# Performance work log

Hardware: AMD Instinct MI355X
Metric: run time of the kernel (lower is better)

The kernel has to match this reference:

```python
import jax, jax.numpy as jnp
import numpy as np

EMBED = 128
HIDDEN = 256
N_NODES = 50000
N_EDGES = 640000
LN_EPS = 1e-5


def setup_inputs() -> dict:
    key = jax.random.key(0)
    ks = jax.random.split(key, 10)
    node_embeddings = jax.random.normal(ks[0], (N_NODES, EMBED), dtype=jnp.float32)
    edge_embeddings = jax.random.normal(ks[1], (N_EDGES, EMBED), dtype=jnp.float32)
    edge_index_list = jax.random.randint(ks[2], (2, N_EDGES), 0, N_NODES, dtype=jnp.int64 if jax.config.jax_enable_x64 else jnp.int32)
    # LayerNorm params
    ln_gamma = jnp.ones((EMBED,), dtype=jnp.float32)
    ln_beta = jnp.zeros((EMBED,), dtype=jnp.float32)
    # phi: Linear(embed->hidden), Linear(hidden->embed); xavier-ish init
    W1 = jax.random.normal(ks[3], (EMBED, HIDDEN), dtype=jnp.float32) * (1.0 / np.sqrt(EMBED))
    b1 = jnp.zeros((HIDDEN,), dtype=jnp.float32)
    W2 = jax.random.normal(ks[4], (HIDDEN, EMBED), dtype=jnp.float32) * (1.0 / np.sqrt(HIDDEN))
    b2 = jnp.zeros((EMBED,), dtype=jnp.float32)
    # theta: Linear(embed->embed)
    Wt = jax.random.normal(ks[5], (EMBED, EMBED), dtype=jnp.float32) * (1.0 / np.sqrt(EMBED))
    bt = jnp.zeros((EMBED,), dtype=jnp.float32)
    return {
        "node_embeddings": node_embeddings,
        "edge_embeddings": edge_embeddings,
        "edge_index_list": edge_index_list,
        "ln_gamma": ln_gamma, "ln_beta": ln_beta,
        "W1": W1, "b1": b1, "W2": W2, "b2": b2,
        "Wt": Wt, "bt": bt,
    }


def _layer_norm(x, gamma, beta):
    mu = jnp.mean(x, axis=-1, keepdims=True)
    var = jnp.var(x, axis=-1, keepdims=True)
    return (x - mu) * jax.lax.rsqrt(var + LN_EPS) * gamma + beta


def reference(node_embeddings, edge_embeddings, edge_index_list,
              ln_gamma, ln_beta, W1, b1, W2, b2, Wt, bt):
    n_nodes = node_embeddings.shape[0]
    h = _layer_norm(node_embeddings, ln_gamma, ln_beta)  # [N, D]
    center = edge_index_list[0]    # [E]
    neighbor = edge_index_list[1]  # [E]
    h_c = h[center]                # [E, D] gather
    h_n = h[neighbor]              # [E, D] gather
    s = edge_embeddings + h_c + h_n  # [E, D]
    # phi: SiLU -> Linear -> SiLU -> Linear
    t = jax.nn.silu(s) @ W1 + b1          # [E, H]
    theta_edge = jax.nn.silu(t) @ W2 + b2  # [E, D]
    msg = h_n * theta_edge                 # [E, D]
    agg = jax.ops.segment_sum(msg, center, num_segments=n_nodes)  # [N, D]
    # theta: SiLU -> Linear
    out = jax.nn.silu(h + agg) @ Wt + bt   # [N, D]
    return out
```

## Files before the change

### kernel.cpp

```cpp
#include <hip/hip_runtime.h>
#include <hip/hip_bf16.h>
#include <stdint.h>

#define EMBED 128
#define HIDDEN 256

typedef __bf16 v8bf __attribute__((ext_vector_type(8)));
typedef float v4f __attribute__((ext_vector_type(4)));

__device__ __forceinline__ float bf2f(unsigned short u){
    union { uint32_t i; float f; } v; v.i = ((uint32_t)u) << 16; return v.f;
}
__device__ __forceinline__ unsigned short f2bf(float f){
    __hip_bfloat16 b = __float2bfloat16(f);
    union { __hip_bfloat16 b; unsigned short u; } cv; cv.b = b; return cv.u;
}
__device__ __forceinline__ uint32_t pack2(float a, float b){
    __hip_bfloat162 t = __float22bfloat162_rn(make_float2(a, b));
    union { __hip_bfloat162 v; uint32_t u; } cv; cv.v = t; return cv.u;
}
__device__ __forceinline__ float lo_f(uint32_t u){ union{uint32_t i;float f;}v; v.i=u<<16; return v.f; }
__device__ __forceinline__ float hi_f(uint32_t u){ union{uint32_t i;float f;}v; v.i=u&0xffff0000u; return v.f; }
__device__ __forceinline__ float silu_f(float x){
    return x * __builtin_amdgcn_rcpf(1.0f + __expf(-x));
}

__device__ __forceinline__ float loadf(const void* b, size_t i, int isf32){
    return isf32 ? ((const float*)b)[i] : bf2f(((const unsigned short*)b)[i]);
}
__device__ __forceinline__ void load8f(const void* base, size_t off, int isf32, float o[8]){
    if (isf32){
        const float* p = (const float*)base + off;
        float4 a = *(const float4*)p, b = *(const float4*)(p + 4);
        o[0]=a.x;o[1]=a.y;o[2]=a.z;o[3]=a.w;o[4]=b.x;o[5]=b.y;o[6]=b.z;o[7]=b.w;
    } else {
        uint4 v = *(const uint4*)((const unsigned short*)base + off);
        uint32_t w[4] = {v.x, v.y, v.z, v.w};
        #pragma unroll
        for (int q = 0; q < 4; q++){ o[2*q] = lo_f(w[q]); o[2*q+1] = hi_f(w[q]); }
    }
}
__device__ __forceinline__ int idx_c(const int* ei, int e, int is64){
    return is64 ? ei[2*(size_t)e] : ei[e];
}
__device__ __forceinline__ int idx_n(const int* ei, int e, int E, int is64){
    return is64 ? ei[2*((size_t)E + e)] : ei[(size_t)E + e];
}

__device__ __forceinline__ int probe_isf32(const void* p, int lane){
    const unsigned short* u = (const unsigned short*)p;
    unsigned short a = u[lane], b = u[64 + lane];
    int bad = (((a >> 7) & 0xFF) >= 0x85) | (((b >> 7) & 0xFF) >= 0x85);
    return __any(bad) ? 1 : 0;
}
__device__ __forceinline__ int probe_is64(const int* ei, int lane){
    int nz = (ei[2*lane + 1] != 0) | (ei[2*(64 + lane) + 1] != 0);
    return __any(nz) ? 0 : 1;
}

__global__ __launch_bounds__(256) void ln_kernel(
    const void* __restrict__ x, const void* __restrict__ g, const void* __restrict__ b,
    unsigned short* __restrict__ h, float* __restrict__ agg, int N)
{
    int wave = threadIdx.x >> 6, lane = threadIdx.x & 63;
    int isf32 = probe_isf32(x, lane);
    int node = blockIdx.x * 4 + wave;
    if (node >= N) return;
    *(float2*)(agg + (size_t)node * EMBED + lane * 2) = make_float2(0.f, 0.f);
    float x0, x1;
    if (isf32){
        float2 v = *(const float2*)((const float*)x + (size_t)node * EMBED + lane * 2);
        x0 = v.x; x1 = v.y;
    } else {
        uint32_t u = *(const uint32_t*)((const unsigned short*)x + (size_t)node * EMBED + lane * 2);
        x0 = lo_f(u); x1 = hi_f(u);
    }
    float s = x0 + x1, ss = x0 * x0 + x1 * x1;
    for (int m = 1; m < 64; m <<= 1){ s += __shfl_xor(s, m); ss += __shfl_xor(ss, m); }
    float mean = s * (1.0f / EMBED);
    float var  = ss * (1.0f / EMBED) - mean * mean;
    float rs   = rsqrtf(var + 1e-5f);
    float g0 = loadf(g, lane * 2, isf32), g1 = loadf(g, lane * 2 + 1, isf32);
    float b0 = loadf(b, lane * 2, isf32), b1v = loadf(b, lane * 2 + 1, isf32);
    float y0 = (x0 - mean) * rs * g0 + b0;
    float y1 = (x1 - mean) * rs * g1 + b1v;
    *(uint32_t*)(h + (size_t)node * EMBED + lane * 2) = pack2(y0, y1);
}

__global__ __launch_bounds__(256) void prepack_kernel(
    const void* __restrict__ W1, const void* __restrict__ W2, const void* __restrict__ Wt,
    const void* __restrict__ b1, const void* __restrict__ b2, const void* __restrict__ bt,
    unsigned short* __restrict__ W1p, unsigned short* __restrict__ W2p,
    unsigned short* __restrict__ Wtp, unsigned short* __restrict__ bpk)
{
    int isf32 = probe_isf32(W1, threadIdx.x & 63);
    int t = blockIdx.x * blockDim.x + threadIdx.x;
    if (t < 32768){
        int j = t & 7, lane = (t >> 3) & 63, k32 = (t >> 9) & 3, nt = t >> 11;
        int k = k32 * 32 + (lane >> 4) * 8 + j, n = nt * 16 + (lane & 15);
        W1p[t] = f2bf(loadf(W1, (size_t)k * HIDDEN + n, isf32));
    } else if (t < 65536){
        int t2 = t - 32768;
        int j = t2 & 7, lane = (t2 >> 3) & 63, k32 = (t2 >> 9) & 7, nt = t2 >> 12;
        int k = k32 * 32 + (lane >> 4) * 8 + j, n = nt * 16 + (lane & 15);
        W2p[t2] = f2bf(loadf(W2, (size_t)k * EMBED + n, isf32));
    } else if (t < 81920){
        int t3 = t - 65536;
        int j = t3 & 7, lane = (t3 >> 3) & 63, k32 = (t3 >> 9) & 3, nt = t3 >> 11;
        int k = k32 * 32 + (lane >> 4) * 8 + j, n = nt * 16 + (lane & 15);
        Wtp[t3] = f2bf(loadf(Wt, (size_t)k * EMBED + n, isf32));
    } else if (t < 82048){
        int i = t - 81920; bpk[i] = f2bf(loadf(b1, i, isf32));
    } else if (t < 82176){
        int i = t - 82048; bpk[128 + i] = f2bf(loadf(b1, 128 + i, isf32));
    } else if (t < 82304){
        int i = t - 82176; bpk[256 + i] = f2bf(loadf(b2, i, isf32));
    } else if (t < 82432){
        int i = t - 82304; bpk[384 + i] = f2bf(loadf(bt, i, isf32));
    }
}

__global__ __launch_bounds__(256, 4) void edge_kernel(
    const void* __restrict__ ee, const unsigned short* __restrict__ h,
    const int* __restrict__ eidx, int E,
    const unsigned short* __restrict__ W1p, const unsigned short* __restrict__ W2p,
    const unsigned short* __restrict__ bpk,
    float* __restrict__ agg)
{
    __shared__ __align__(16) unsigned short sbuf[64][136];
    __shared__ __align__(16) unsigned short tbuf[64][136];
    __shared__ int cbuf[64], nbuf[64];
    int wave = threadIdx.x >> 6, lane = threadIdx.x & 63;
    int quad = lane >> 4, l16 = lane & 15;
    int isf32 = probe_isf32(ee, lane);
    int is64  = probe_is64(eidx, lane);
    int ebase = blockIdx.x * 64;
    int colg = l16 * 8;

    #pragma unroll
    for (int i = 0; i < 4; i++){
        int row = wave * 16 + i * 4 + quad;
        int e = ebase + row; if (e >= E) e = E - 1;
        int c = idx_c(eidx, e, is64), n = idx_n(eidx, e, E, is64);
        if (l16 == 0){ cbuf[row] = c; nbuf[row] = n; }
        float fe[8];
        load8f(ee, (size_t)e * EMBED + colg, isf32, fe);
        uint4 vc = *(const uint4*)(h + (size_t)c * EMBED + colg);
        uint4 vn = *(const uint4*)(h + (size_t)n * EMBED + colg);
        uint32_t pc[4] = {vc.x, vc.y, vc.z, vc.w};
        uint32_t pn[4] = {vn.x, vn.y, vn.z, vn.w};
        uint32_t o[4];
        #pragma unroll
        for (int q = 0; q < 4; q++){
            float a0 = fe[2*q]   + lo_f(pc[q]) + lo_f(pn[q]);
            float a1 = fe[2*q+1] + hi_f(pc[q]) + hi_f(pn[q]);
            o[q] = pack2(silu_f(a0), silu_f(a1));
        }
        *(uint4*)&sbuf[row][colg] = make_uint4(o[0], o[1], o[2], o[3]);
    }
    __syncthreads();

    v4f acc2[4][2];
    {
        float bias2[2];
        #pragma unroll
        for (int j = 0; j < 2; j++) bias2[j] = bf2f(bpk[256 + (wave * 2 + j) * 16 + l16]);
        #pragma unroll
        for (int rt = 0; rt < 4; rt++)
            #pragma unroll
            for (int j = 0; j < 2; j++)
                acc2[rt][j] = (v4f){bias2[j], bias2[j], bias2[j], bias2[j]};
    }

    #pragma unroll
    for (int hf = 0; hf < 2; hf++){
        {
            int ntb = hf * 8 + wave * 2;
            v8bf bw[2][4];
            float bias[2];
            #pragma unroll
            for (int j = 0; j < 2; j++){
                bias[j] = bf2f(bpk[(ntb + j) * 16 + l16]);
                #pragma unroll
                for (int k32 = 0; k32 < 4; k32++)
                    bw[j][k32] = *(const v8bf*)(W1p + ((size_t)((ntb + j) * 4 + k32) * 64 + lane) * 8);
            }
            #pragma unroll
            for (int rt = 0; rt < 4; rt++){
                v8bf a[4];
                #pragma unroll
                for (int k32 = 0; k32 < 4; k32++)
                    a[k32] = *(const v8bf*)&sbuf[rt * 16 + l16][k32 * 32 + quad * 8];
                v4f acc[2];
                #pragma unroll
                for (int j = 0; j < 2; j++) acc[j] = (v4f){bias[j], bias[j], bias[j], bias[j]};
                #pragma unroll
                for (int k32 = 0; k32 < 4; k32++)
                    #pragma unroll
                    for (int j = 0; j < 2; j++)
                        acc[j] = __builtin_amdgcn_mfma_f32_16x16x32_bf16(a[k32], bw[j][k32], acc[j], 0, 0, 0);
                #pragma unroll
                for (int j = 0; j < 2; j++)
                    #pragma unroll
                    for (int r = 0; r < 4; r++)
                        tbuf[rt * 16 + quad * 4 + r][(wave * 2 + j) * 16 + l16] = f2bf(silu_f(acc[j][r]));
            }
        }
        __syncthreads();
        {
            v8bf bw2[2][4];
            #pragma unroll
            for (int j = 0; j < 2; j++)
                #pragma unroll
                for (int kk = 0; kk < 4; kk++)
                    bw2[j][kk] = *(const v8bf*)(W2p + ((size_t)((wave * 2 + j) * 8 + hf * 4 + kk) * 64 + lane) * 8);
            #pragma unroll
            for (int rt = 0; rt < 4; rt++){
                v8bf a[4];
                #pragma unroll
                for (int kk = 0; kk < 4; kk++)
                    a[kk] = *(const v8bf*)&tbuf[rt * 16 + l16][kk * 32 + quad * 8];
                #pragma unroll
                for (int kk = 0; kk < 4; kk++)
                    #pragma unroll
                    for (int j = 0; j < 2; j++)
                        acc2[rt][j] = __builtin_amdgcn_mfma_f32_16x16x32_bf16(a[kk], bw2[j][kk], acc2[rt][j], 0, 0, 0);
            }
        }
        if (hf == 0) __syncthreads();
    }

    #pragma unroll
    for (int rt = 0; rt < 4; rt++){
        #pragma unroll
        for (int r = 0; r < 4; r++){
            int row = rt * 16 + quad * 4 + r;
            int e = ebase + row;
            if (e < E){
                int c = cbuf[row], n = nbuf[row];
                #pragma unroll
                for (int j = 0; j < 2; j++){
                    int col = (wave * 2 + j) * 16 + l16;
                    float hn = bf2f(h[(size_t)n * EMBED + col]);
                    atomicAdd(&agg[(size_t)c * EMBED + col], acc2[rt][j][r] * hn);
                }
            }
        }
    }
}

__global__ __launch_bounds__(256) void node_out_kernel(
    const void* __restrict__ ne,
    const unsigned short* __restrict__ h, const float* __restrict__ agg,
    const unsigned short* __restrict__ Wtp, const unsigned short* __restrict__ bpk,
    void* __restrict__ out, int N)
{
    __shared__ __align__(16) unsigned short ubuf[4][16][136];
    int wave = threadIdx.x >> 6, lane = threadIdx.x & 63;
    int isf32 = probe_isf32(ne, lane);
    int quad = lane >> 4, l16 = lane & 15;
    int nbase = (blockIdx.x * 4 + wave) * 16;
    int colg = l16 * 8;
    #pragma unroll
    for (int i = 0; i < 4; i++){
        int row = i * 4 + quad;
        int node = nbase + row; int nn = node < N ? node : N - 1;
        uint4 vh = *(const uint4*)(h + (size_t)nn * EMBED + colg);
        float4 a0 = *(const float4*)(agg + (size_t)nn * EMBED + colg);
        float4 a1 = *(const float4*)(agg + (size_t)nn * EMBED + colg + 4);
        uint32_t ph[4] = {vh.x, vh.y, vh.z, vh.w};
        float af[8] = {a0.x, a0.y, a0.z, a0.w, a1.x, a1.y, a1.z, a1.w};
        uint32_t o[4];
        #pragma unroll
        for (int q = 0; q < 4; q++){
            float u0 = lo_f(ph[q]) + af[2 * q];
            float u1 = hi_f(ph[q]) + af[2 * q + 1];
            o[q] = pack2(silu_f(u0), silu_f(u1));
        }
        *(uint4*)&ubuf[wave][row][colg] = make_uint4(o[0], o[1], o[2], o[3]);
    }
    __syncthreads();
    for (int nt = 0; nt < 8; nt++){
        int col = nt * 16 + l16;
        float bc = bf2f(bpk[384 + col]);
        v4f acc = {bc, bc, bc, bc};
        #pragma unroll
        for (int k32 = 0; k32 < 4; k32++){
            v8bf a = *(const v8bf*)&ubuf[wave][l16][k32 * 32 + quad * 8];
            v8bf b = *(const v8bf*)(Wtp + ((size_t)(nt * 4 + k32) * 64 + lane) * 8);
            acc = __builtin_amdgcn_mfma_f32_16x16x32_bf16(a, b, acc, 0, 0, 0);
        }
        #pragma unroll
        for (int r = 0; r < 4; r++){
            int node = nbase + quad * 4 + r;
            if (node < N){
                if (isf32) ((float*)out)[(size_t)node * EMBED + col] = acc[r];
                else ((unsigned short*)out)[(size_t)node * EMBED + col] = f2bf(acc[r]);
            }
        }
    }
}

extern "C" void kernel_launch(void* const* d_in, const int* in_sizes, int n_in,
                              void* d_out, int out_size, void* d_ws, size_t ws_size,
                              hipStream_t stream)
{
    const void* ne = d_in[0];
    const void* ee = d_in[1];
    const int* eidx = (const int*)d_in[2];
    const void* g  = d_in[3];
    const void* be = d_in[4];
    const void* W1 = d_in[5];
    const void* b1 = d_in[6];
    const void* W2 = d_in[7];
    const void* b2 = d_in[8];
    const void* Wt = d_in[9];
    const void* bt = d_in[10];
    int N = in_sizes[0] / EMBED;
    int E = in_sizes[2] / 2;

    char* ws = (char*)d_ws;
    unsigned short* h = (unsigned short*)ws;
    float* agg = (float*)(ws + (size_t)N * EMBED * 2);
    unsigned short* W1p = (unsigned short*)(ws + (size_t)N * EMBED * 2 + (size_t)N * EMBED * 4);
    unsigned short* W2p = W1p + 32768;
    unsigned short* Wtp = W2p + 32768;
    unsigned short* bpk = Wtp + 16384;

    prepack_kernel<<<(82432 + 255) / 256, 256, 0, stream>>>(W1, W2, Wt, b1, b2, bt,
                                                            W1p, W2p, Wtp, bpk);
    ln_kernel<<<(N + 3) / 4, 256, 0, stream>>>(ne, g, be, h, agg, N);
    edge_kernel<<<(E + 63) / 64, 256, 0, stream>>>(ee, h, eidx, E,
                                                   W1p, W2p, bpk, agg);
    node_out_kernel<<<(N + 63) / 64, 256, 0, stream>>>(ne, h, agg, Wtp, bpk,
                                                       d_out, N);
}
```

Measured before the change: 782.9 us.

## Sort edges by center node and segment-reduce messages before writing

Adds a counting sort of edges by center index: a histogram kernel, a single-block scan and an atomic scatter that produce a permutation plus sorted center and neighbor arrays. The edge kernel reads edges in sorted order. It stages messages in shared memory that reuses the sbuf/tbuf space, then reduces runs of equal centers per column. Only boundary segments use atomicAdd, and fully contained segments use plain stores. This removes most of the per-element global float atomics, at the cost of three extra launches, a memset, a serial single-block scan, and an indirect gather of edge embeddings.

```diff
diff --git a/kernel.cpp b/kernel.cpp
--- a/kernel.cpp
+++ b/kernel.cpp
@@ -56,6 +56,54 @@
 __device__ __forceinline__ int probe_is64(const int* ei, int lane){
     int nz = (ei[2*lane + 1] != 0) | (ei[2*(64 + lane) + 1] != 0);
     return __any(nz) ? 0 : 1;
+}
+
+__global__ __launch_bounds__(256) void hist_kernel(
+    const int* __restrict__ eidx, int E, int* __restrict__ cnt)
+{
+    int is64 = probe_is64(eidx, threadIdx.x & 63);
+    int e = blockIdx.x * 256 + threadIdx.x;
+    if (e < E) atomicAdd(&cnt[idx_c(eidx, e, is64)], 1);
+}
+
+__global__ __launch_bounds__(1024) void scan_kernel(
+    const int* __restrict__ cnt, int* __restrict__ cur, int N)
+{
+    __shared__ int wpart[16];
+    int t = threadIdx.x;
+    int Cg = (N + 1023) >> 10;
+    int base = t * Cg;
+    int s = 0;
+    for (int i = 0; i < Cg; i++){ int k = base + i; if (k < N) s += cnt[k]; }
+    int lane = t & 63, w = t >> 6;
+    int x = s;
+    for (int m = 1; m < 64; m <<= 1){ int y = __shfl_up(x, m); if (lane >= m) x += y; }
+    if (lane == 63) wpart[w] = x;
+    __syncthreads();
+    if (t < 16){
+        int v = wpart[t];
+        for (int m = 1; m < 16; m <<= 1){ int y = __shfl_up(v, m); if (t >= m) v += y; }
+        wpart[t] = v;
+    }
+    __syncthreads();
+    int excl = x - s + (w ? wpart[w - 1] : 0);
+    for (int i = 0; i < Cg; i++){
+        int k = base + i;
+        if (k < N){ cur[k] = excl; excl += cnt[k]; }
+    }
+}
+
+__global__ __launch_bounds__(256) void scatter_kernel(
+    const int* __restrict__ eidx, int E, int* __restrict__ cur,
+    int* __restrict__ eid, int* __restrict__ cs, int* __restrict__ ns)
+{
+    int is64 = probe_is64(eidx, threadIdx.x & 63);
+    int e = blockIdx.x * 256 + threadIdx.x;
+    if (e < E){
+        int c = idx_c(eidx, e, is64), n = idx_n(eidx, e, E, is64);
+        int p = atomicAdd(&cur[c], 1);
+        eid[p] = e; cs[p] = c; ns[p] = n;
+    }
 }
 
 __global__ __launch_bounds__(256) void ln_kernel(
@@ -122,26 +170,29 @@
 
 __global__ __launch_bounds__(256, 4) void edge_kernel(
     const void* __restrict__ ee, const unsigned short* __restrict__ h,
-    const int* __restrict__ eidx, int E,
+    const int* __restrict__ eid, const int* __restrict__ cs, const int* __restrict__ ns,
+    int E,
     const unsigned short* __restrict__ W1p, const unsigned short* __restrict__ W2p,
     const unsigned short* __restrict__ bpk,
     float* __restrict__ agg)
 {
-    __shared__ __align__(16) unsigned short sbuf[64][136];
-    __shared__ __align__(16) unsigned short tbuf[64][136];
+    __shared__ __align__(16) unsigned short sraw[64 * 136 * 2];
     __shared__ int cbuf[64], nbuf[64];
+    unsigned short (*sbuf)[136] = (unsigned short (*)[136])sraw;
+    unsigned short (*tbuf)[136] = (unsigned short (*)[136])(sraw + 64 * 136);
+    float* msg = (float*)sraw;
+
     int wave = threadIdx.x >> 6, lane = threadIdx.x & 63;
     int quad = lane >> 4, l16 = lane & 15;
     int isf32 = probe_isf32(ee, lane);
-    int is64  = probe_is64(eidx, lane);
     int ebase = blockIdx.x * 64;
     int colg = l16 * 8;
 
     #pragma unroll
     for (int i = 0; i < 4; i++){
         int row = wave * 16 + i * 4 + quad;
-        int e = ebase + row; if (e >= E) e = E - 1;
-        int c = idx_c(eidx, e, is64), n = idx_n(eidx, e, E, is64);
+        int sp = ebase + row; if (sp >= E) sp = E - 1;
+        int e = eid[sp], c = cs[sp], n = ns[sp];
         if (l16 == 0){ cbuf[row] = c; nbuf[row] = n; }
         float fe[8];
         load8f(ee, (size_t)e * EMBED + colg, isf32, fe);
@@ -227,25 +278,47 @@
                         acc2[rt][j] = __builtin_amdgcn_mfma_f32_16x16x32_bf16(a[kk], bw2[j][kk], acc2[rt][j], 0, 0, 0);
             }
         }
-        if (hf == 0) __syncthreads();
+        __syncthreads();
     }
 
     #pragma unroll
     for (int rt = 0; rt < 4; rt++){
         #pragma unroll
-        for (int r = 0; r < 4; r++){
-            int row = rt * 16 + quad * 4 + r;
-            int e = ebase + row;
-            if (e < E){
-                int c = cbuf[row], n = nbuf[row];
-                #pragma unroll
-                for (int j = 0; j < 2; j++){
-                    int col = (wave * 2 + j) * 16 + l16;
-                    float hn = bf2f(h[(size_t)n * EMBED + col]);
-                    atomicAdd(&agg[(size_t)c * EMBED + col], acc2[rt][j][r] * hn);
+        for (int j = 0; j < 2; j++){
+            int col = (wave * 2 + j) * 16 + l16;
+            #pragma unroll
+            for (int r = 0; r < 4; r++){
+                int row = rt * 16 + quad * 4 + r;
+                int n = nbuf[row];
+                float hn = bf2f(h[(size_t)n * EMBED + col]);
+                msg[row * 132 + col] = acc2[rt][j][r] * hn;
+            }
+        }
+    }
+    __syncthreads();
+
+    {
+        int col  = threadIdx.x & 127;
+        int half = threadIdx.x >> 7;
+        int r0 = half * 32;
+        float acc = 0.f;
+        int ccur = -1;
+        int first = 1;
+        for (int row = r0; row < r0 + 32; ++row){
+            if (ebase + row >= E) break;
+            int c = cbuf[row];
+            if (c != ccur){
+                if (ccur >= 0){
+                    if (first) atomicAdd(&agg[(size_t)ccur * EMBED + col], acc);
+                    else       agg[(size_t)ccur * EMBED + col] = acc;
+                    first = 0;
                 }
-            }
-        }
+                ccur = c; acc = 0.f;
+            }
+            acc += msg[row * 132 + col];
+        }
+        if (ccur >= 0)
+            atomicAdd(&agg[(size_t)ccur * EMBED + col], acc);
     }
 }
 
@@ -320,17 +393,32 @@
     int E = in_sizes[2] / 2;
 
     char* ws = (char*)d_ws;
-    unsigned short* h = (unsigned short*)ws;
-    float* agg = (float*)(ws + (size_t)N * EMBED * 2);
-    unsigned short* W1p = (unsigned short*)(ws + (size_t)N * EMBED * 2 + (size_t)N * EMBED * 4);
-    unsigned short* W2p = W1p + 32768;
-    unsigned short* Wtp = W2p + 32768;
-    unsigned short* bpk = Wtp + 16384;
-
+    size_t off = 0;
+    unsigned short* h = (unsigned short*)(ws + off); off += (size_t)N * EMBED * 2;
+    off = (off + 255) & ~(size_t)255;
+    float* agg = (float*)(ws + off);                 off += (size_t)N * EMBED * 4;
+    off = (off + 255) & ~(size_t)255;
+    unsigned short* W1p = (unsigned short*)(ws + off); off += 32768 * 2;
+    unsigned short* W2p = (unsigned short*)(ws + off); off += 32768 * 2;
+    unsigned short* Wtp = (unsigned short*)(ws + off); off += 16384 * 2;
+    unsigned short* bpk = (unsigned short*)(ws + off); off += 512 * 2;
+    off = (off + 255) & ~(size_t)255;
+    int* cnt = (int*)(ws + off); off += (size_t)N * 4;
+    off = (off + 255) & ~(size_t)255;
+    int* cur = (int*)(ws + off); off += (size_t)N * 4;
+    off = (off + 255) & ~(size_t)255;
+    int* eid = (int*)(ws + off); off += (size_t)E * 4;
+    int* cs  = (int*)(ws + off); off += (size_t)E * 4;
+    int* ns  = (int*)(ws + off); off += (size_t)E * 4;
+
+    hipMemsetAsync(cnt, 0, (size_t)N * 4, stream);
     prepack_kernel<<<(82432 + 255) / 256, 256, 0, stream>>>(W1, W2, Wt, b1, b2, bt,
                                                             W1p, W2p, Wtp, bpk);
+    hist_kernel<<<(E + 255) / 256, 256, 0, stream>>>(eidx, E, cnt);
+    scan_kernel<<<1, 1024, 0, stream>>>(cnt, cur, N);
+    scatter_kernel<<<(E + 255) / 256, 256, 0, stream>>>(eidx, E, cur, eid, cs, ns);
     ln_kernel<<<(N + 3) / 4, 256, 0, stream>>>(ne, g, be, h, agg, N);
-    edge_kernel<<<(E + 63) / 64, 256, 0, stream>>>(ee, h, eidx, E,
+    edge_kernel<<<(E + 63) / 64, 256, 0, stream>>>(ee, h, eid, cs, ns, E,
                                                    W1p, W2p, bpk, agg);
     node_out_kernel<<<(N + 63) / 64, 256, 0, stream>>>(ne, h, agg, Wtp, bpk,
                                                        d_out, N);
```

Result: no change. 781.7 us (-0.1%).
